# Performance work log

Measured on AMD Instinct MI355X. Metric: run time of the kernel, lower is better.

Reference implementation:

```python
import jax, jax.numpy as jnp
import numpy as np

N_SEG = 16384      # number of ragged segments (customers)
SEG_LEN = 1024     # events per segment (uniform here; math supports ragged)
N = N_SEG * SEG_LEN
EPS = 1e-5


def setup_inputs() -> dict:
    key = jax.random.key(0)
    k1, k2 = jax.random.split(key)
    # tau = detached model prediction of next inter-event time; must be > 0
    tau = jax.random.uniform(k1, (N,), jnp.float32, 0.1, 2.0)
    # dt = observed inter-event times (non-negative)
    dt = jax.random.uniform(k2, (N,), jnp.float32, 0.0, 1.0)
    # offsets: B+1 boundaries of the ragged segments within the flat arrays
    offsets = jnp.arange(N_SEG + 1, dtype=jnp.int32) * SEG_LEN
    return {"tau": tau, "dt": dt, "offsets": offsets}


def reference(tau, dt, offsets):
    # Original loop: per segment, drop first and last event, accumulate
    # -log_prob under Exponential(rate=1/tau):
    #   -log_prob(x) = log(tau) + (dt + eps) / tau
    # Replaced by a single masked elementwise pass + sum: interior mask is
    # everything except each segment's first index and last index.
    n = dt.shape[0]
    mask = (
        jnp.ones((n,), dtype=bool)
        .at[offsets[:-1]].set(False)      # segment starts
        .at[offsets[1:] - 1].set(False)   # segment ends
    )
    tau_sg = jax.lax.stop_gradient(tau)   # y_pred['next_dt'].detach()
    nll = jnp.log(tau_sg) + (dt + EPS) / tau_sg
    loss = jnp.sum(jnp.where(mask, nll, jnp.zeros((), nll.dtype)))
    final_loss = loss / offsets.shape[0]  # divide by B+1, as in source
    return final_loss
```

## Files before the change

kernel.cpp:

```cpp
#include <hip/hip_runtime.h>

#define EPS 1e-5f
#define THREADS 256
#define MAIN_BLOCKS 2048
#define SUPER 2048
#define BND_THREADS 256

__global__ __launch_bounds__(THREADS, 2) void tau_loss_main(
    const float4* __restrict__ t4,
    const float4* __restrict__ d4,
    const float* __restrict__ tau,
    const float* __restrict__ dt,
    float* __restrict__ ws,
    int n) {
    const int n4 = n >> 2;
    const int nsuper = n4 / SUPER;

    float a0 = 0.f, a1 = 0.f, a2 = 0.f, a3 = 0.f;

    for (int s = blockIdx.x; s < nsuper; s += MAIN_BLOCKS) {
        const int base = s * SUPER + (int)threadIdx.x;
        float4 t0 = t4[base + 0 * THREADS];
        float4 e0 = d4[base + 0 * THREADS];
        float4 t1 = t4[base + 1 * THREADS];
        float4 e1 = d4[base + 1 * THREADS];
        float4 t2 = t4[base + 2 * THREADS];
        float4 e2 = d4[base + 2 * THREADS];
        float4 t3 = t4[base + 3 * THREADS];
        float4 e3 = d4[base + 3 * THREADS];
        float4 t4v = t4[base + 4 * THREADS];
        float4 e4 = d4[base + 4 * THREADS];
        float4 t5 = t4[base + 5 * THREADS];
        float4 e5 = d4[base + 5 * THREADS];
        float4 t6 = t4[base + 6 * THREADS];
        float4 e6 = d4[base + 6 * THREADS];
        float4 t7 = t4[base + 7 * THREADS];
        float4 e7 = d4[base + 7 * THREADS];
        a0 += __logf(t0.x) + __fdividef(e0.x + EPS, t0.x);
        a1 += __logf(t0.y) + __fdividef(e0.y + EPS, t0.y);
        a2 += __logf(t0.z) + __fdividef(e0.z + EPS, t0.z);
        a3 += __logf(t0.w) + __fdividef(e0.w + EPS, t0.w);
        a0 += __logf(t1.x) + __fdividef(e1.x + EPS, t1.x);
        a1 += __logf(t1.y) + __fdividef(e1.y + EPS, t1.y);
        a2 += __logf(t1.z) + __fdividef(e1.z + EPS, t1.z);
        a3 += __logf(t1.w) + __fdividef(e1.w + EPS, t1.w);
        a0 += __logf(t2.x) + __fdividef(e2.x + EPS, t2.x);
        a1 += __logf(t2.y) + __fdividef(e2.y + EPS, t2.y);
        a2 += __logf(t2.z) + __fdividef(e2.z + EPS, t2.z);
        a3 += __logf(t2.w) + __fdividef(e2.w + EPS, t2.w);
        a0 += __logf(t3.x) + __fdividef(e3.x + EPS, t3.x);
        a1 += __logf(t3.y) + __fdividef(e3.y + EPS, t3.y);
        a2 += __logf(t3.z) + __fdividef(e3.z + EPS, t3.z);
        a3 += __logf(t3.w) + __fdividef(e3.w + EPS, t3.w);
        a0 += __logf(t4v.x) + __fdividef(e4.x + EPS, t4v.x);
        a1 += __logf(t4v.y) + __fdividef(e4.y + EPS, t4v.y);
        a2 += __logf(t4v.z) + __fdividef(e4.z + EPS, t4v.z);
        a3 += __logf(t4v.w) + __fdividef(e4.w + EPS, t4v.w);
        a0 += __logf(t5.x) + __fdividef(e5.x + EPS, t5.x);
        a1 += __logf(t5.y) + __fdividef(e5.y + EPS, t5.y);
        a2 += __logf(t5.z) + __fdividef(e5.z + EPS, t5.z);
        a3 += __logf(t5.w) + __fdividef(e5.w + EPS, t5.w);
        a0 += __logf(t6.x) + __fdividef(e6.x + EPS, t6.x);
        a1 += __logf(t6.y) + __fdividef(e6.y + EPS, t6.y);
        a2 += __logf(t6.z) + __fdividef(e6.z + EPS, t6.z);
        a3 += __logf(t6.w) + __fdividef(e6.w + EPS, t6.w);
        a0 += __logf(t7.x) + __fdividef(e7.x + EPS, t7.x);
        a1 += __logf(t7.y) + __fdividef(e7.y + EPS, t7.y);
        a2 += __logf(t7.z) + __fdividef(e7.z + EPS, t7.z);
        a3 += __logf(t7.w) + __fdividef(e7.w + EPS, t7.w);
    }

    if (blockIdx.x == 0) {
        for (int i = nsuper * (SUPER * 4) + (int)threadIdx.x; i < n; i += THREADS) {
            float t = tau[i];
            a0 += __logf(t) + __fdividef(dt[i] + EPS, t);
        }
    }

    float acc = (a0 + a1) + (a2 + a3);

    #pragma unroll
    for (int off = 32; off > 0; off >>= 1)
        acc += __shfl_down(acc, off, 64);

    __shared__ float smem[THREADS / 64];
    int wave = threadIdx.x >> 6;
    int lane = threadIdx.x & 63;
    if (lane == 0) smem[wave] = acc;
    __syncthreads();
    if (threadIdx.x == 0)
        ws[blockIdx.x] = smem[0] + smem[1] + smem[2] + smem[3];
}

__global__ __launch_bounds__(BND_THREADS) void tau_loss_boundary(
    const float* __restrict__ tau,
    const float* __restrict__ dt,
    const int* __restrict__ offsets,
    float* __restrict__ ws,
    int nseg) {
    int k = blockIdx.x * blockDim.x + threadIdx.x;

    float sub = 0.0f;
    if (k < nseg) {
        int s = offsets[k];
        int e = offsets[k + 1] - 1;
        float ts = tau[s];
        sub = __logf(ts) + __fdividef(dt[s] + EPS, ts);
        if (e != s) {
            float te = tau[e];
            sub += __logf(te) + __fdividef(dt[e] + EPS, te);
        }
    }

    #pragma unroll
    for (int off = 32; off > 0; off >>= 1)
        sub += __shfl_down(sub, off, 64);

    __shared__ float smem[BND_THREADS / 64];
    int wave = threadIdx.x >> 6;
    int lane = threadIdx.x & 63;
    if (lane == 0) smem[wave] = sub;
    __syncthreads();
    if (threadIdx.x == 0)
        ws[MAIN_BLOCKS + blockIdx.x] = -(smem[0] + smem[1] + smem[2] + smem[3]);
}

__global__ __launch_bounds__(256) void tau_loss_final(
    const float* __restrict__ ws, int m, float inv_div,
    float* __restrict__ out) {
    float a = 0.f;
    for (int i = threadIdx.x; i < m; i += 256)
        a += ws[i];

    #pragma unroll
    for (int off = 32; off > 0; off >>= 1)
        a += __shfl_down(a, off, 64);

    __shared__ float smem[4];
    int wave = threadIdx.x >> 6;
    int lane = threadIdx.x & 63;
    if (lane == 0) smem[wave] = a;
    __syncthreads();
    if (threadIdx.x == 0)
        out[0] = (smem[0] + smem[1] + smem[2] + smem[3]) * inv_div;
}

extern "C" void kernel_launch(void* const* d_in, const int* in_sizes, int n_in,
                              void* d_out, int out_size, void* d_ws, size_t ws_size,
                              hipStream_t stream) {
    const float* tau = (const float*)d_in[0];
    const float* dt  = (const float*)d_in[1];
    const int* offsets = (const int*)d_in[2];
    float* out = (float*)d_out;
    float* ws = (float*)d_ws;

    const int n = in_sizes[0];
    const int n_off = in_sizes[2];
    const int nseg = n_off - 1;
    const float inv_div = 1.0f / (float)n_off;

    tau_loss_main<<<MAIN_BLOCKS, THREADS, 0, stream>>>(
        (const float4*)tau, (const float4*)dt, tau, dt, ws, n);

    int bblocks = (nseg + BND_THREADS - 1) / BND_THREADS;
    if (bblocks < 1) bblocks = 1;
    tau_loss_boundary<<<bblocks, BND_THREADS, 0, stream>>>(tau, dt, offsets, ws, nseg);

    tau_loss_final<<<1, 256, 0, stream>>>(ws, MAIN_BLOCKS + bblocks, inv_div, out);
}
```

Before: 34.22 us.

## Double-buffer main loop loads with inline asm and explicit vmcnt waits

Replaces the main reduction loop with a software-pipelined, double-buffered scheme. Loads are issued through inline global_load_dwordx4 asm, with staged s_waitcnt vmcnt waits, so the next super-tile's loads are in flight while the current one is computed. This aims to hide memory latency in a bandwidth-bound reduction. It doubles the vector registers used for staging, which may reduce occupancy, and inline asm loads bypass compiler scheduling, which carries correctness risk.

New measurement: 32.82 us. 1.04x faster.

```diff
diff --git a/kernel.cpp b/kernel.cpp
--- a/kernel.cpp
+++ b/kernel.cpp
@@ -1,4 +1,6 @@
 #include <hip/hip_runtime.h>
+
+typedef float f32x4 __attribute__((ext_vector_type(4)));
 
 #define EPS 1e-5f
 #define THREADS 256
@@ -6,9 +8,44 @@
 #define SUPER 2048
 #define BND_THREADS 256
 
+#define GLOAD(dst, addr) \
+  asm volatile("global_load_dwordx4 %0, %1, off" : "=v"(dst) : "v"(addr) : "memory")
+
+#define SWAIT(n) \
+  asm volatile("s_waitcnt vmcnt(" #n ")" ::: "memory"); \
+  __builtin_amdgcn_sched_barrier(0)
+
+#define NLL4(T, E) \
+  a0 += __logf(T.x) + __fdividef(E.x + EPS, T.x); \
+  a1 += __logf(T.y) + __fdividef(E.y + EPS, T.y); \
+  a2 += __logf(T.z) + __fdividef(E.z + EPS, T.z); \
+  a3 += __logf(T.w) + __fdividef(E.w + EPS, T.w)
+
+#define ISSUE(T, E, P, Q) \
+  GLOAD(T##0, P + 0 * THREADS); GLOAD(E##0, Q + 0 * THREADS); \
+  GLOAD(T##1, P + 1 * THREADS); GLOAD(E##1, Q + 1 * THREADS); \
+  GLOAD(T##2, P + 2 * THREADS); GLOAD(E##2, Q + 2 * THREADS); \
+  GLOAD(T##3, P + 3 * THREADS); GLOAD(E##3, Q + 3 * THREADS); \
+  GLOAD(T##4, P + 4 * THREADS); GLOAD(E##4, Q + 4 * THREADS); \
+  GLOAD(T##5, P + 5 * THREADS); GLOAD(E##5, Q + 5 * THREADS); \
+  GLOAD(T##6, P + 6 * THREADS); GLOAD(E##6, Q + 6 * THREADS); \
+  GLOAD(T##7, P + 7 * THREADS); GLOAD(E##7, Q + 7 * THREADS)
+
+#define COMPUTE16(T, E) \
+  SWAIT(28); NLL4(T##0, E##0); NLL4(T##1, E##1); \
+  SWAIT(24); NLL4(T##2, E##2); NLL4(T##3, E##3); \
+  SWAIT(20); NLL4(T##4, E##4); NLL4(T##5, E##5); \
+  SWAIT(16); NLL4(T##6, E##6); NLL4(T##7, E##7)
+
+#define COMPUTE0(T, E) \
+  SWAIT(12); NLL4(T##0, E##0); NLL4(T##1, E##1); \
+  SWAIT(8);  NLL4(T##2, E##2); NLL4(T##3, E##3); \
+  SWAIT(4);  NLL4(T##4, E##4); NLL4(T##5, E##5); \
+  SWAIT(0);  NLL4(T##6, E##6); NLL4(T##7, E##7)
+
 __global__ __launch_bounds__(THREADS, 2) void tau_loss_main(
-    const float4* __restrict__ t4,
-    const float4* __restrict__ d4,
+    const f32x4* __restrict__ t4,
+    const f32x4* __restrict__ d4,
     const float* __restrict__ tau,
     const float* __restrict__ dt,
     float* __restrict__ ws,
@@ -18,56 +55,37 @@
 
     float a0 = 0.f, a1 = 0.f, a2 = 0.f, a3 = 0.f;
 
-    for (int s = blockIdx.x; s < nsuper; s += MAIN_BLOCKS) {
-        const int base = s * SUPER + (int)threadIdx.x;
-        float4 t0 = t4[base + 0 * THREADS];
-        float4 e0 = d4[base + 0 * THREADS];
-        float4 t1 = t4[base + 1 * THREADS];
-        float4 e1 = d4[base + 1 * THREADS];
-        float4 t2 = t4[base + 2 * THREADS];
-        float4 e2 = d4[base + 2 * THREADS];
-        float4 t3 = t4[base + 3 * THREADS];
-        float4 e3 = d4[base + 3 * THREADS];
-        float4 t4v = t4[base + 4 * THREADS];
-        float4 e4 = d4[base + 4 * THREADS];
-        float4 t5 = t4[base + 5 * THREADS];
-        float4 e5 = d4[base + 5 * THREADS];
-        float4 t6 = t4[base + 6 * THREADS];
-        float4 e6 = d4[base + 6 * THREADS];
-        float4 t7 = t4[base + 7 * THREADS];
-        float4 e7 = d4[base + 7 * THREADS];
-        a0 += __logf(t0.x) + __fdividef(e0.x + EPS, t0.x);
-        a1 += __logf(t0.y) + __fdividef(e0.y + EPS, t0.y);
-        a2 += __logf(t0.z) + __fdividef(e0.z + EPS, t0.z);
-        a3 += __logf(t0.w) + __fdividef(e0.w + EPS, t0.w);
-        a0 += __logf(t1.x) + __fdividef(e1.x + EPS, t1.x);
-        a1 += __logf(t1.y) + __fdividef(e1.y + EPS, t1.y);
-        a2 += __logf(t1.z) + __fdividef(e1.z + EPS, t1.z);
-        a3 += __logf(t1.w) + __fdividef(e1.w + EPS, t1.w);
-        a0 += __logf(t2.x) + __fdividef(e2.x + EPS, t2.x);
-        a1 += __logf(t2.y) + __fdividef(e2.y + EPS, t2.y);
-        a2 += __logf(t2.z) + __fdividef(e2.z + EPS, t2.z);
-        a3 += __logf(t2.w) + __fdividef(e2.w + EPS, t2.w);
-        a0 += __logf(t3.x) + __fdividef(e3.x + EPS, t3.x);
-        a1 += __logf(t3.y) + __fdividef(e3.y + EPS, t3.y);
-        a2 += __logf(t3.z) + __fdividef(e3.z + EPS, t3.z);
-        a3 += __logf(t3.w) + __fdividef(e3.w + EPS, t3.w);
-        a0 += __logf(t4v.x) + __fdividef(e4.x + EPS, t4v.x);
-        a1 += __logf(t4v.y) + __fdividef(e4.y + EPS, t4v.y);
-        a2 += __logf(t4v.z) + __fdividef(e4.z + EPS, t4v.z);
-        a3 += __logf(t4v.w) + __fdividef(e4.w + EPS, t4v.w);
-        a0 += __logf(t5.x) + __fdividef(e5.x + EPS, t5.x);
-        a1 += __logf(t5.y) + __fdividef(e5.y + EPS, t5.y);
-        a2 += __logf(t5.z) + __fdividef(e5.z + EPS, t5.z);
-        a3 += __logf(t5.w) + __fdividef(e5.w + EPS, t5.w);
-        a0 += __logf(t6.x) + __fdividef(e6.x + EPS, t6.x);
-        a1 += __logf(t6.y) + __fdividef(e6.y + EPS, t6.y);
-        a2 += __logf(t6.z) + __fdividef(e6.z + EPS, t6.z);
-        a3 += __logf(t6.w) + __fdividef(e6.w + EPS, t6.w);
-        a0 += __logf(t7.x) + __fdividef(e7.x + EPS, t7.x);
-        a1 += __logf(t7.y) + __fdividef(e7.y + EPS, t7.y);
-        a2 += __logf(t7.z) + __fdividef(e7.z + EPS, t7.z);
-        a3 += __logf(t7.w) + __fdividef(e7.w + EPS, t7.w);
+    f32x4 tA0, tA1, tA2, tA3, tA4, tA5, tA6, tA7;
+    f32x4 eA0, eA1, eA2, eA3, eA4, eA5, eA6, eA7;
+    f32x4 tB0, tB1, tB2, tB3, tB4, tB5, tB6, tB7;
+    f32x4 eB0, eB1, eB2, eB3, eB4, eB5, eB6, eB7;
+
+    int s = (int)blockIdx.x;
+    if (s < nsuper) {
+        const f32x4* pt = t4 + s * SUPER + (int)threadIdx.x;
+        const f32x4* pe = d4 + s * SUPER + (int)threadIdx.x;
+        ISSUE(tA, eA, pt, pe);
+        s += MAIN_BLOCKS;
+
+        while (s < nsuper) {
+            pt = t4 + s * SUPER + (int)threadIdx.x;
+            pe = d4 + s * SUPER + (int)threadIdx.x;
+            ISSUE(tB, eB, pt, pe);
+            COMPUTE16(tA, eA);
+            s += MAIN_BLOCKS;
+            if (s < nsuper) {
+                pt = t4 + s * SUPER + (int)threadIdx.x;
+                pe = d4 + s * SUPER + (int)threadIdx.x;
+                ISSUE(tA, eA, pt, pe);
+                COMPUTE16(tB, eB);
+                s += MAIN_BLOCKS;
+            } else {
+                COMPUTE0(tB, eB);
+                goto main_done;
+            }
+        }
+        COMPUTE0(tA, eA);
+        main_done: ;
     }
 
     if (blockIdx.x == 0) {
@@ -160,7 +178,7 @@
     const float inv_div = 1.0f / (float)n_off;
 
     tau_loss_main<<<MAIN_BLOCKS, THREADS, 0, stream>>>(
-        (const float4*)tau, (const float4*)dt, tau, dt, ws, n);
+        (const f32x4*)tau, (const f32x4*)dt, tau, dt, ws, n);
 
     int bblocks = (nseg + BND_THREADS - 1) / BND_THREADS;
     if (bblocks < 1) bblocks = 1;
```
